# Kernel tuning notes

Hardware: AMD Instinct MI355X
Metric: run time of the kernel (lower is better)

## Reference

```python
import jax, jax.numpy as jnp
import numpy as np

B, N, K, H, C = 16, 2048, 9, 128, 2  # K = nb_neighbors, kernel_size = K+1


def setup_inputs() -> dict:
    key = jax.random.key(0)
    ks = jax.random.split(key, 7)
    s = 0.1
    x = jax.random.normal(ks[0], (B, N, C), jnp.float32)
    Wconv = jax.random.normal(ks[1], (H, C, K + 1), jnp.float32) * s  # conv1d weight
    bconv = jax.random.normal(ks[2], (H,), jnp.float32) * s
    W1 = jax.random.normal(ks[3], (H, C), jnp.float32) * s
    b1 = jax.random.normal(ks[4], (H,), jnp.float32) * s
    W2 = jax.random.normal(ks[5], (H, H), jnp.float32) * s
    b2 = jax.random.normal(ks[6], (H,), jnp.float32) * s
    return {"x": x, "Wconv": Wconv, "bconv": bconv, "W1": W1, "b1": b1, "W2": W2, "b2": b2}


def reference(x, Wconv, bconv, W1, b1, W2, b2):
    # node embedding: W1(x)
    node_emb = jnp.einsum('bnc,hc->bnh', x, W1) + b1  # (B,N,H)

    # pairwise Euclidean distances (B,N,N) via the GEMM form
    sq = jnp.sum(x * x, axis=-1)  # (B,N)
    d2 = sq[:, :, None] + sq[:, None, :] - 2.0 * jnp.einsum('bnc,bmc->bnm', x, x)
    dist = jnp.sqrt(jnp.maximum(d2, 0.0))

    # torch: topk(k=N) (descending) then take last K+1 columns -> the K+1
    # smallest distances ordered descending (nearest/self last)
    knn = jnp.flip(jnp.argsort(dist, axis=-1)[..., : K + 1], axis=-1)  # (B,N,K+1)

    # batched gather of neighbor coords: (B,N,K+1,C)
    coords = jax.vmap(lambda xb, ib: xb[ib])(x, knn)

    # conv1d with kernel spanning the full window -> single output position,
    # i.e. a contraction over (channel, position)
    conv_emb = jnp.einsum('bnkc,hck->bnh', coords, Wconv) + bconv  # (B,N,H)
    conv_emb = jnp.einsum('bnh,eh->bne', conv_emb, W2) + b2

    return node_emb + conv_emb
```

## Files before the change

### kernel.cpp

```cpp
#include <hip/hip_runtime.h>
#include <cfloat>
#include <stdint.h>

#define B_   16
#define N_   2048
#define KK   10
#define H_   128
#define SUB  32
#define NCH  (N_ / SUB)

__device__ inline uint32_t f32_ordered(float f) {
    uint32_t u = __float_as_uint(f);
    return (u & 0x80000000u) ? ~u : (u | 0x80000000u);
}

__global__ __launch_bounds__(1024) void setup_kernel(
    const float* __restrict__ x,
    const float* __restrict__ Wconv, const float* __restrict__ bconv,
    const float* __restrict__ b1,    const float* __restrict__ W2,
    const float* __restrict__ b2,
    float4* __restrict__ xsorted,
    float*  __restrict__ weff,
    float*  __restrict__ btot)
{
#pragma clang fp contract(off)
    __shared__ uint64_t sk[N_];
    const int tid = threadIdx.x;
    if (blockIdx.x >= 16) {
        int gid = (blockIdx.x - 16) * 1024 + tid;
        if (gid < H_ * KK * 2) {
            int e = gid / 20, r = gid % 20, k = r >> 1, c = r & 1;
            float acc = 0.f;
            for (int h = 0; h < H_; ++h)
                acc += W2[e * H_ + h] * Wconv[h * (2 * KK) + c * KK + k];
            weff[gid] = acc;
        } else if (gid < H_ * KK * 2 + H_) {
            int e = gid - H_ * KK * 2;
            float acc = b1[e] + b2[e];
            for (int h = 0; h < H_; ++h) acc += W2[e * H_ + h] * bconv[h];
            btot[e] = acc;
        }
        return;
    }
    const int b = blockIdx.x;
    const float2* xb = (const float2*)(x + (size_t)b * N_ * 2);
    for (int i = tid; i < N_; i += 1024)
        sk[i] = ((uint64_t)f32_ordered(xb[i].x) << 32) | (uint32_t)i;
    __syncthreads();
    for (int size = 2; size <= N_; size <<= 1) {
        for (int stride = size >> 1; stride > 0; stride >>= 1) {
            int i = 2 * tid - (tid & (stride - 1));
            int j = i + stride;
            bool up = ((i & size) == 0);
            uint64_t a = sk[i], c = sk[j];
            if (up ? (a > c) : (a < c)) { sk[i] = c; sk[j] = a; }
            __syncthreads();
        }
    }
    for (int i = tid; i < N_; i += 1024) {
        uint32_t idx = (uint32_t)sk[i];
        float2 p = xb[idx];
        float sm = p.x * p.x + p.y * p.y;
        xsorted[(size_t)b * N_ + i] = make_float4(p.x, p.y, sm, __uint_as_float(idx));
    }
}

__global__ __launch_bounds__(512, 4) void knn_conv_kernel(
    const float4* __restrict__ xsorted,
    const float* __restrict__ W1,
    const float* __restrict__ weff,
    const float* __restrict__ btot,
    float* __restrict__ out)
{
#pragma clang fp contract(off)
    __shared__ float4   xs4[N_];
    __shared__ uint64_t mkeys[64 * 81];
    __shared__ float    wcoord[64 * 21];

    const int tid  = threadIdx.x;
    const int w    = tid >> 6;
    const int l    = tid & 63;
    const int b    = blockIdx.x >> 5;
    const int tile = blockIdx.x & 31;

    const float4* xb = xsorted + (size_t)b * N_;
    for (int i = tid; i < N_; i += 512) xs4[i] = xb[i];
    __syncthreads();

    const int    n  = tile * 64 + l;
    const float4 qv = xs4[n];
    const float  qx = qv.x, qy = qv.y, sqn = qv.z;
    const float  qa  = xs4[tile * 64].x;
    const float  qbx = xs4[tile * 64 + 63].x;

    const uint64_t KINIT = (((uint64_t)0x7F7FFFFFu) << 32) | 0x3FFFFFu;
    uint64_t hk[KK];
#pragma unroll
    for (int j = 0; j < KK; ++j) hk[j] = KINIT;
    float h9d = FLT_MAX;

    auto scan_chunk = [&](int mc) {
        for (int mm = 0; mm < SUB; ++mm) {
            const int m = mc + mm;
            float4 c4 = xs4[m];
            float s  = sqn + c4.z;
            float pr = qx * c4.x;
            float dt = __builtin_fmaf(qy, c4.y, pr);
            float d2 = __builtin_fmaf(-2.0f, dt, s);
            float dc = d2 > 0.0f ? d2 : 0.0f;
            if (dc <= h9d) {
                uint32_t oi = __float_as_uint(c4.w);
                uint64_t key = ((uint64_t)__float_as_uint(dc) << 32)
                             | (oi << 11) | (uint32_t)m;
                if (key < hk[KK - 1]) {
#pragma unroll
                    for (int j = KK - 1; j >= 1; --j) {
                        bool cj  = key < hk[j];
                        bool cjm = key < hk[j - 1];
                        hk[j] = cj ? (cjm ? hk[j - 1] : key) : hk[j];
                    }
                    hk[0] = (key < hk[0]) ? key : hk[0];
                }
                h9d = __uint_as_float((uint32_t)(hk[KK - 1] >> 32));
            }
        }
    };

    const int ct2 = 2 * tile;
    const int a   = (w - ct2) & 7;
    const int c1  = ct2 + a;
    const int c2  = c1 - 8;
    int c_near = (a <= 4) ? c1 : c2;
    if (c1 > NCH - 1) c_near = c2;
    if (c2 < 0)       c_near = c1;
    scan_chunk(c_near * SUB);

    int  cl = c_near - 8, cr = c_near + 8;
    bool la = (cl >= 0), ra = (cr <= NCH - 1);
    while (la || ra) {
        float wm = h9d;
        wm = fmaxf(wm, __shfl_xor(wm, 1,  64));
        wm = fmaxf(wm, __shfl_xor(wm, 2,  64));
        wm = fmaxf(wm, __shfl_xor(wm, 4,  64));
        wm = fmaxf(wm, __shfl_xor(wm, 8,  64));
        wm = fmaxf(wm, __shfl_xor(wm, 16, 64));
        wm = fmaxf(wm, __shfl_xor(wm, 32, 64));
        float gl = la ? (qa - xs4[cl * SUB + SUB - 1].x) : FLT_MAX;
        float gr = ra ? (xs4[cr * SUB].x - qbx)          : FLT_MAX;
        bool pickL = la && (!ra || gl <= gr);
        if (pickL) {
            if (__builtin_fmaf(gl, gl, -4e-6f) > wm) la = false;
            else { scan_chunk(cl * SUB); cl -= 8; la = (cl >= 0); }
        } else {
            if (__builtin_fmaf(gr, gr, -4e-6f) > wm) ra = false;
            else { scan_chunk(cr * SUB); cr += 8; ra = (cr <= NCH - 1); }
        }
    }

    {
        const int mb = l * 81 + w * 10;
#pragma unroll
        for (int j = 0; j < KK; ++j) mkeys[mb + j] = hk[j];
    }

    const int e = tid & 127;
    float we[20];
    {
        const float4* wp = (const float4*)(weff + e * 20);
#pragma unroll
        for (int r = 0; r < 5; ++r) {
            float4 v = wp[r];
            we[4 * r + 0] = v.x; we[4 * r + 1] = v.y;
            we[4 * r + 2] = v.z; we[4 * r + 3] = v.w;
        }
    }
    const float w1x = W1[e * 2 + 0];
    const float w1y = W1[e * 2 + 1];
    const float bt  = btot[e];
    __syncthreads();

    {
        const int q = tid >> 3;
        const int r = tid & 7;
        const int mb = q * 81 + r * 10;
        int p = 0;
#pragma unroll
        for (int sel = 0; sel < KK; ++sel) {
            uint64_t v = (p < KK) ? mkeys[mb + p] : 0xFFFFFFFFFFFFFFFFull;
            uint64_t t1 = __shfl_xor((unsigned long long)v, 1, 64);
            uint64_t m1 = v  < t1 ? v  : t1;
            uint64_t t2 = __shfl_xor((unsigned long long)m1, 2, 64);
            uint64_t m2 = m1 < t2 ? m1 : t2;
            uint64_t t4 = __shfl_xor((unsigned long long)m2, 4, 64);
            uint64_t vm = m2 < t4 ? m2 : t4;
            if (v == vm) {
                ++p;
                float4 c = xs4[(int)(vm & 0x7FF)];
                const int k = (KK - 1) - sel;
                wcoord[q * 21 + 2 * k + 0] = c.x;
                wcoord[q * 21 + 2 * k + 1] = c.y;
            }
        }
    }
    __syncthreads();

    const int qb_ = tid >> 7;
    const size_t obase = (size_t)b * N_ * H_;
#pragma unroll
    for (int jj = 0; jj < 16; ++jj) {
        const int qq = qb_ + 4 * jj;
        float4 xq = xs4[tile * 64 + qq];
        uint32_t orig = __float_as_uint(xq.w);
        const float* wc = &wcoord[qq * 21];
        float acc = bt;
        acc += xq.x * w1x;
        acc += xq.y * w1y;
#pragma unroll
        for (int k = 0; k < KK; ++k) {
            acc += wc[2 * k + 0] * we[2 * k + 0];
            acc += wc[2 * k + 1] * we[2 * k + 1];
        }
        out[obase + (size_t)orig * H_ + e] = acc;
    }
}

extern "C" void kernel_launch(void* const* d_in, const int* in_sizes, int n_in,
                              void* d_out, int out_size, void* d_ws, size_t ws_size,
                              hipStream_t stream) {
    const float* x     = (const float*)d_in[0];
    const float* Wconv = (const float*)d_in[1];
    const float* bconv = (const float*)d_in[2];
    const float* W1    = (const float*)d_in[3];
    const float* b1    = (const float*)d_in[4];
    const float* W2    = (const float*)d_in[5];
    const float* b2    = (const float*)d_in[6];
    float* out  = (float*)d_out;
    float* weff = (float*)d_ws;
    float* btot = weff + H_ * KK * 2;
    float4* xsorted = (float4*)((char*)d_ws + 16384);

    setup_kernel<<<dim3(19), dim3(1024), 0, stream>>>(
        x, Wconv, bconv, b1, W2, b2, xsorted, weff, btot);
    knn_conv_kernel<<<dim3(B_ * (N_ / 64)), dim3(512), 0, stream>>>(
        xsorted, W1, weff, btot, out);
}
```

Before: 161.8 us.

## Assign eight lanes per query with per-lane sorted-x pruning over 16-point chunks

Reworks the kNN search so each query is handled by 8 adjacent lanes, each scanning interleaved 16-point chunks of the x-sorted points. Early termination now uses the query's own x-gap against a bound shared among its 8 lanes, replacing the wavefront-wide max reduction and the greedy left/right loop. The per-lane top-10 lists are merged directly through register shuffles, which removes the shared mkeys buffer and one barrier. The pruning bound is taken only after the first chunk and is never tightened, so some lanes may scan more chunks than before.

```diff
diff --git a/kernel.cpp b/kernel.cpp
--- a/kernel.cpp
+++ b/kernel.cpp
@@ -6,7 +6,7 @@
 #define N_   2048
 #define KK   10
 #define H_   128
-#define SUB  32
+#define SUB  16
 #define NCH  (N_ / SUB)
 
 __device__ inline uint32_t f32_ordered(float f) {
@@ -65,6 +65,8 @@
     }
 }
 
+#define KINIT ((((uint64_t)0x7F800000u) << 32) | 0xFFFFFFFFull)
+
 __global__ __launch_bounds__(512, 4) void knn_conv_kernel(
     const float4* __restrict__ xsorted,
     const float* __restrict__ W1,
@@ -73,13 +75,12 @@
     float* __restrict__ out)
 {
 #pragma clang fp contract(off)
-    __shared__ float4   xs4[N_];
-    __shared__ uint64_t mkeys[64 * 81];
-    __shared__ float    wcoord[64 * 21];
+    __shared__ float4 xs4[N_];
+    __shared__ float  wcoord[64 * 21];
 
     const int tid  = threadIdx.x;
-    const int w    = tid >> 6;
-    const int l    = tid & 63;
+    const int qi   = tid >> 3;
+    const int ri   = tid & 7;
     const int b    = blockIdx.x >> 5;
     const int tile = blockIdx.x & 31;
 
@@ -87,31 +88,28 @@
     for (int i = tid; i < N_; i += 512) xs4[i] = xb[i];
     __syncthreads();
 
-    const int    n  = tile * 64 + l;
+    const int    n  = tile * 64 + qi;
     const float4 qv = xs4[n];
     const float  qx = qv.x, qy = qv.y, sqn = qv.z;
-    const float  qa  = xs4[tile * 64].x;
-    const float  qbx = xs4[tile * 64 + 63].x;
-
-    const uint64_t KINIT = (((uint64_t)0x7F7FFFFFu) << 32) | 0x3FFFFFu;
+
     uint64_t hk[KK];
 #pragma unroll
     for (int j = 0; j < KK; ++j) hk[j] = KINIT;
-    float h9d = FLT_MAX;
-
-    auto scan_chunk = [&](int mc) {
+    float h9f = __uint_as_float(0x7F800000u);
+
+    auto scan16 = [&](int c) {
+        const int base = c << 4;
         for (int mm = 0; mm < SUB; ++mm) {
-            const int m = mc + mm;
-            float4 c4 = xs4[m];
+            float4 c4 = xs4[base + mm];
             float s  = sqn + c4.z;
             float pr = qx * c4.x;
             float dt = __builtin_fmaf(qy, c4.y, pr);
             float d2 = __builtin_fmaf(-2.0f, dt, s);
             float dc = d2 > 0.0f ? d2 : 0.0f;
-            if (dc <= h9d) {
+            if (dc <= h9f) {
                 uint32_t oi = __float_as_uint(c4.w);
                 uint64_t key = ((uint64_t)__float_as_uint(dc) << 32)
-                             | (oi << 11) | (uint32_t)m;
+                             | (oi << 11) | (uint32_t)(base + mm);
                 if (key < hk[KK - 1]) {
 #pragma unroll
                     for (int j = KK - 1; j >= 1; --j) {
@@ -120,47 +118,37 @@
                         hk[j] = cj ? (cjm ? hk[j - 1] : key) : hk[j];
                     }
                     hk[0] = (key < hk[0]) ? key : hk[0];
+                    h9f = __uint_as_float((uint32_t)(hk[KK - 1] >> 32));
                 }
-                h9d = __uint_as_float((uint32_t)(hk[KK - 1] >> 32));
             }
         }
     };
 
-    const int ct2 = 2 * tile;
-    const int a   = (w - ct2) & 7;
-    const int c1  = ct2 + a;
-    const int c2  = c1 - 8;
-    int c_near = (a <= 4) ? c1 : c2;
-    if (c1 > NCH - 1) c_near = c2;
-    if (c2 < 0)       c_near = c1;
-    scan_chunk(c_near * SUB);
-
-    int  cl = c_near - 8, cr = c_near + 8;
-    bool la = (cl >= 0), ra = (cr <= NCH - 1);
-    while (la || ra) {
-        float wm = h9d;
-        wm = fmaxf(wm, __shfl_xor(wm, 1,  64));
-        wm = fmaxf(wm, __shfl_xor(wm, 2,  64));
-        wm = fmaxf(wm, __shfl_xor(wm, 4,  64));
-        wm = fmaxf(wm, __shfl_xor(wm, 8,  64));
-        wm = fmaxf(wm, __shfl_xor(wm, 16, 64));
-        wm = fmaxf(wm, __shfl_xor(wm, 32, 64));
-        float gl = la ? (qa - xs4[cl * SUB + SUB - 1].x) : FLT_MAX;
-        float gr = ra ? (xs4[cr * SUB].x - qbx)          : FLT_MAX;
-        bool pickL = la && (!ra || gl <= gr);
-        if (pickL) {
-            if (__builtin_fmaf(gl, gl, -4e-6f) > wm) la = false;
-            else { scan_chunk(cl * SUB); cl -= 8; la = (cl >= 0); }
-        } else {
-            if (__builtin_fmaf(gr, gr, -4e-6f) > wm) ra = false;
-            else { scan_chunk(cr * SUB); cr += 8; ra = (cr <= NCH - 1); }
-        }
-    }
-
-    {
-        const int mb = l * 81 + w * 10;
-#pragma unroll
-        for (int j = 0; j < KK; ++j) mkeys[mb + j] = hk[j];
+    const int T0 = 4 * tile;
+    int cb_ = T0 + ((ri - T0) & 7);
+    int ca_ = cb_ - 8;
+    int cn;
+    if (cb_ <= T0 + 3) cn = cb_;
+    else cn = ((T0 - ca_) < (cb_ - (T0 + 3))) ? ca_ : cb_;
+    if (cn < 0)    cn = cb_;
+    if (cn >= NCH) cn = ca_;
+    scan16(cn);
+
+    float qb = h9f;
+    qb = fminf(qb, __shfl_xor(qb, 1, 64));
+    qb = fminf(qb, __shfl_xor(qb, 2, 64));
+    qb = fminf(qb, __shfl_xor(qb, 4, 64));
+    const float qbm = qb + 1e-7f;
+
+    for (int c = cn - 8; c >= 0; c -= 8) {
+        float gap = qx - xs4[(c << 4) + 15].x;
+        if (gap * gap > qbm) break;
+        scan16(c);
+    }
+    for (int c = cn + 8; c < NCH; c += 8) {
+        float gap = fmaxf(0.0f, xs4[c << 4].x - qx);
+        if (gap * gap > qbm) break;
+        scan16(c);
     }
 
     const int e = tid & 127;
@@ -177,29 +165,23 @@
     const float w1x = W1[e * 2 + 0];
     const float w1y = W1[e * 2 + 1];
     const float bt  = btot[e];
-    __syncthreads();
-
-    {
-        const int q = tid >> 3;
-        const int r = tid & 7;
-        const int mb = q * 81 + r * 10;
-        int p = 0;
-#pragma unroll
-        for (int sel = 0; sel < KK; ++sel) {
-            uint64_t v = (p < KK) ? mkeys[mb + p] : 0xFFFFFFFFFFFFFFFFull;
-            uint64_t t1 = __shfl_xor((unsigned long long)v, 1, 64);
-            uint64_t m1 = v  < t1 ? v  : t1;
-            uint64_t t2 = __shfl_xor((unsigned long long)m1, 2, 64);
-            uint64_t m2 = m1 < t2 ? m1 : t2;
-            uint64_t t4 = __shfl_xor((unsigned long long)m2, 4, 64);
-            uint64_t vm = m2 < t4 ? m2 : t4;
-            if (v == vm) {
-                ++p;
-                float4 c = xs4[(int)(vm & 0x7FF)];
-                const int k = (KK - 1) - sel;
-                wcoord[q * 21 + 2 * k + 0] = c.x;
-                wcoord[q * 21 + 2 * k + 1] = c.y;
-            }
+
+#pragma unroll
+    for (int sel = 0; sel < KK; ++sel) {
+        uint64_t v = hk[0], t;
+        t = __shfl_xor((unsigned long long)v, 1, 64); v = (t < v) ? t : v;
+        t = __shfl_xor((unsigned long long)v, 2, 64); v = (t < v) ? t : v;
+        t = __shfl_xor((unsigned long long)v, 4, 64); v = (t < v) ? t : v;
+        if (ri == (sel & 7)) {
+            float4 c = xs4[(int)(v & 0x7FF)];
+            const int k = (KK - 1) - sel;
+            wcoord[qi * 21 + 2 * k + 0] = c.x;
+            wcoord[qi * 21 + 2 * k + 1] = c.y;
+        }
+        if (hk[0] == v) {
+#pragma unroll
+            for (int j = 0; j < KK - 1; ++j) hk[j] = hk[j + 1];
+            hk[KK - 1] = KINIT;
         }
     }
     __syncthreads();
```

Result: slower. 191.2 us (+18.2%).

## Use branchless float top-K threshold pass then exact capture rescan

Applied to the files above, without the earlier changes.

The KNN search kernel now uses 4 waves of 256 threads with 16-point chunks. The first pass keeps a branchless min/max sorting network over float distances only, without the divergent 64-bit key insertion. A second rescan of the visited chunks captures candidates at or below the threshold into a small per-thread shared buffer, where they are sorted with exact tie-break keys. Points are read straight from global/L2 instead of being staged in shared memory, which saves LDS and the initial copy. The cost is a second distance pass, more global traffic, and a correctness risk if more than 12 candidates tie at the threshold.

```diff
diff --git a/kernel.cpp b/kernel.cpp
--- a/kernel.cpp
+++ b/kernel.cpp
@@ -6,8 +6,10 @@
 #define N_   2048
 #define KK   10
 #define H_   128
-#define SUB  32
+#define SUB  16
 #define NCH  (N_ / SUB)
+#define W_   4
+#define CAP  12
 
 __device__ inline uint32_t f32_ordered(float f) {
     uint32_t u = __float_as_uint(f);
@@ -65,7 +67,9 @@
     }
 }
 
-__global__ __launch_bounds__(512, 4) void knn_conv_kernel(
+#define KINIT 0xFFFFFFFFFFFFFFFFull
+
+__global__ __launch_bounds__(256, 4) void knn_conv_kernel(
     const float4* __restrict__ xsorted,
     const float* __restrict__ W1,
     const float* __restrict__ weff,
@@ -73,94 +77,145 @@
     float* __restrict__ out)
 {
 #pragma clang fp contract(off)
-    __shared__ float4   xs4[N_];
-    __shared__ uint64_t mkeys[64 * 81];
+    __shared__ uint64_t cap[W_ * 64 * 13];
+    __shared__ uint32_t poslist[64 * KK];
     __shared__ float    wcoord[64 * 21];
 
     const int tid  = threadIdx.x;
     const int w    = tid >> 6;
-    const int l    = tid & 63;
+    const int qi   = tid & 63;
     const int b    = blockIdx.x >> 5;
     const int tile = blockIdx.x & 31;
 
     const float4* xb = xsorted + (size_t)b * N_;
-    for (int i = tid; i < N_; i += 512) xs4[i] = xb[i];
-    __syncthreads();
-
-    const int    n  = tile * 64 + l;
-    const float4 qv = xs4[n];
+    const int    n  = tile * 64 + qi;
+    const float4 qv = xb[n];
     const float  qx = qv.x, qy = qv.y, sqn = qv.z;
-    const float  qa  = xs4[tile * 64].x;
-    const float  qbx = xs4[tile * 64 + 63].x;
-
-    const uint64_t KINIT = (((uint64_t)0x7F7FFFFFu) << 32) | 0x3FFFFFu;
-    uint64_t hk[KK];
-#pragma unroll
-    for (int j = 0; j < KK; ++j) hk[j] = KINIT;
-    float h9d = FLT_MAX;
-
-    auto scan_chunk = [&](int mc) {
+    const float  txa = xb[tile * 64].x;
+    const float  txb = xb[tile * 64 + 63].x;
+
+    float hd[KK];
+#pragma unroll
+    for (int j = 0; j < KK; ++j) hd[j] = FLT_MAX;
+
+    auto dist = [&](float4 c4) -> float {
+        float s  = sqn + c4.z;
+        float pr = qx * c4.x;
+        float dt = __builtin_fmaf(qy, c4.y, pr);
+        float d2 = __builtin_fmaf(-2.0f, dt, s);
+        return d2 > 0.0f ? d2 : 0.0f;
+    };
+
+    auto scan1 = [&](int c) {
+        const float4* cp = xb + (c << 4);
+#pragma unroll
         for (int mm = 0; mm < SUB; ++mm) {
-            const int m = mc + mm;
-            float4 c4 = xs4[m];
-            float s  = sqn + c4.z;
-            float pr = qx * c4.x;
-            float dt = __builtin_fmaf(qy, c4.y, pr);
-            float d2 = __builtin_fmaf(-2.0f, dt, s);
-            float dc = d2 > 0.0f ? d2 : 0.0f;
-            if (dc <= h9d) {
-                uint32_t oi = __float_as_uint(c4.w);
-                uint64_t key = ((uint64_t)__float_as_uint(dc) << 32)
-                             | (oi << 11) | (uint32_t)m;
-                if (key < hk[KK - 1]) {
-#pragma unroll
-                    for (int j = KK - 1; j >= 1; --j) {
-                        bool cj  = key < hk[j];
-                        bool cjm = key < hk[j - 1];
-                        hk[j] = cj ? (cjm ? hk[j - 1] : key) : hk[j];
-                    }
-                    hk[0] = (key < hk[0]) ? key : hk[0];
-                }
-                h9d = __uint_as_float((uint32_t)(hk[KK - 1] >> 32));
+            float v = dist(cp[mm]);
+            float prev = hd[0];
+            hd[0] = fminf(v, hd[0]);
+#pragma unroll
+            for (int j = 1; j < KK; ++j) {
+                float cur = hd[j];
+                hd[j] = fmaxf(prev, fminf(v, cur));
+                prev = cur;
             }
         }
     };
 
-    const int ct2 = 2 * tile;
-    const int a   = (w - ct2) & 7;
-    const int c1  = ct2 + a;
-    const int c2  = c1 - 8;
-    int c_near = (a <= 4) ? c1 : c2;
-    if (c1 > NCH - 1) c_near = c2;
-    if (c2 < 0)       c_near = c1;
-    scan_chunk(c_near * SUB);
-
-    int  cl = c_near - 8, cr = c_near + 8;
-    bool la = (cl >= 0), ra = (cr <= NCH - 1);
+    const int c0 = 4 * tile + w;
+    scan1(c0);
+    int clo = c0, chi = c0;
+
+    int  cl = c0 - 4, cr = c0 + 4;
+    bool la = (cl >= 0), ra = (cr < NCH);
     while (la || ra) {
-        float wm = h9d;
+        float wm = hd[KK - 1];
         wm = fmaxf(wm, __shfl_xor(wm, 1,  64));
         wm = fmaxf(wm, __shfl_xor(wm, 2,  64));
         wm = fmaxf(wm, __shfl_xor(wm, 4,  64));
         wm = fmaxf(wm, __shfl_xor(wm, 8,  64));
         wm = fmaxf(wm, __shfl_xor(wm, 16, 64));
         wm = fmaxf(wm, __shfl_xor(wm, 32, 64));
-        float gl = la ? (qa - xs4[cl * SUB + SUB - 1].x) : FLT_MAX;
-        float gr = ra ? (xs4[cr * SUB].x - qbx)          : FLT_MAX;
+        float gl = la ? fmaxf(0.0f, txa - xb[(cl << 4) + 15].x) : FLT_MAX;
+        float gr = ra ? fmaxf(0.0f, xb[cr << 4].x - txb)        : FLT_MAX;
         bool pickL = la && (!ra || gl <= gr);
         if (pickL) {
-            if (__builtin_fmaf(gl, gl, -4e-6f) > wm) la = false;
-            else { scan_chunk(cl * SUB); cl -= 8; la = (cl >= 0); }
+            if (gl * gl - 4e-6f > wm) la = false;
+            else { scan1(cl); clo = cl; cl -= 4; la = (cl >= 0); }
         } else {
-            if (__builtin_fmaf(gr, gr, -4e-6f) > wm) ra = false;
-            else { scan_chunk(cr * SUB); cr += 8; ra = (cr <= NCH - 1); }
-        }
-    }
+            if (gr * gr - 4e-6f > wm) ra = false;
+            else { scan1(cr); chi = cr; cr += 4; ra = (cr < NCH); }
+        }
+    }
+
+    const float tau = hd[KK - 1];
+
+    const int cb = (w * 64 + qi) * 13;
+#pragma unroll
+    for (int i = 0; i < CAP; ++i) cap[cb + i] = KINIT;
+    int cnt = 0;
+    for (int c = clo; c <= chi; c += 4) {
+        const float4* cp = xb + (c << 4);
+#pragma unroll
+        for (int mm = 0; mm < SUB; ++mm) {
+            float4 c4 = cp[mm];
+            float v = dist(c4);
+            if (v <= tau) {
+                if (cnt < CAP) {
+                    uint32_t oi = __float_as_uint(c4.w);
+                    uint64_t key = ((uint64_t)__float_as_uint(v) << 32)
+                                 | (oi << 11) | (uint32_t)((c << 4) + mm);
+                    cap[cb + cnt] = key;
+                }
+                ++cnt;
+            }
+        }
+    }
+
+    uint64_t hk[KK];
+#pragma unroll
+    for (int j = 0; j < KK; ++j) hk[j] = KINIT;
+#pragma unroll
+    for (int i = 0; i < CAP; ++i) {
+        uint64_t key = cap[cb + i];
+        if (key < hk[KK - 1]) {
+#pragma unroll
+            for (int j = KK - 1; j >= 1; --j) {
+                bool cj  = key < hk[j];
+                bool cjm = key < hk[j - 1];
+                hk[j] = cj ? (cjm ? hk[j - 1] : key) : hk[j];
+            }
+            hk[0] = (key < hk[0]) ? key : hk[0];
+        }
+    }
+#pragma unroll
+    for (int j = 0; j < KK; ++j) cap[cb + j] = hk[j];
+    __syncthreads();
 
     {
-        const int mb = l * 81 + w * 10;
-#pragma unroll
-        for (int j = 0; j < KK; ++j) mkeys[mb + j] = hk[j];
+        const int q = tid >> 2;
+        const int r = tid & 3;
+        int p = 0;
+#pragma unroll
+        for (int sel = 0; sel < KK; ++sel) {
+            uint64_t v = (p < KK) ? cap[(r * 64 + q) * 13 + p] : KINIT;
+            uint64_t t;
+            t = __shfl_xor((unsigned long long)v, 1, 64); v = (t < v) ? t : v;
+            uint64_t vm = v;
+            t = __shfl_xor((unsigned long long)vm, 2, 64); vm = (t < vm) ? t : vm;
+            uint64_t own = (p < KK) ? cap[(r * 64 + q) * 13 + p] : KINIT;
+            if (r == 0) poslist[q * KK + sel] = (uint32_t)(vm & 0x7FF);
+            if (own == vm) ++p;
+        }
+    }
+    __syncthreads();
+
+    for (int i = tid; i < 64 * KK; i += 256) {
+        int q   = i / KK;
+        int sel = i - q * KK;
+        float4 c4 = xb[poslist[i]];
+        wcoord[q * 21 + 2 * (KK - 1 - sel) + 0] = c4.x;
+        wcoord[q * 21 + 2 * (KK - 1 - sel) + 1] = c4.y;
     }
 
     const int e = tid & 127;
@@ -179,37 +234,12 @@
     const float bt  = btot[e];
     __syncthreads();
 
-    {
-        const int q = tid >> 3;
-        const int r = tid & 7;
-        const int mb = q * 81 + r * 10;
-        int p = 0;
-#pragma unroll
-        for (int sel = 0; sel < KK; ++sel) {
-            uint64_t v = (p < KK) ? mkeys[mb + p] : 0xFFFFFFFFFFFFFFFFull;
-            uint64_t t1 = __shfl_xor((unsigned long long)v, 1, 64);
-            uint64_t m1 = v  < t1 ? v  : t1;
-            uint64_t t2 = __shfl_xor((unsigned long long)m1, 2, 64);
-            uint64_t m2 = m1 < t2 ? m1 : t2;
-            uint64_t t4 = __shfl_xor((unsigned long long)m2, 4, 64);
-            uint64_t vm = m2 < t4 ? m2 : t4;
-            if (v == vm) {
-                ++p;
-                float4 c = xs4[(int)(vm & 0x7FF)];
-                const int k = (KK - 1) - sel;
-                wcoord[q * 21 + 2 * k + 0] = c.x;
-                wcoord[q * 21 + 2 * k + 1] = c.y;
-            }
-        }
-    }
-    __syncthreads();
-
-    const int qb_ = tid >> 7;
+    const int half = tid >> 7;
     const size_t obase = (size_t)b * N_ * H_;
-#pragma unroll
-    for (int jj = 0; jj < 16; ++jj) {
-        const int qq = qb_ + 4 * jj;
-        float4 xq = xs4[tile * 64 + qq];
+#pragma unroll 4
+    for (int jj = 0; jj < 32; ++jj) {
+        const int qq = half + 2 * jj;
+        float4 xq = xb[tile * 64 + qq];
         uint32_t orig = __float_as_uint(xq.w);
         const float* wc = &wcoord[qq * 21];
         float acc = bt;
@@ -241,6 +271,6 @@
 
     setup_kernel<<<dim3(19), dim3(1024), 0, stream>>>(
         x, Wconv, bconv, b1, W2, b2, xsorted, weff, btot);
-    knn_conv_kernel<<<dim3(B_ * (N_ / 64)), dim3(512), 0, stream>>>(
+    knn_conv_kernel<<<dim3(B_ * 32), dim3(256), 0, stream>>>(
         xsorted, W1, weff, btot, out);
 }
```

After: 208.6 us. +29.0%, slower.
